# Kernel tuning notes

Hardware: AMD Instinct MI355X
Metric: run time of the kernel (lower is better)

The kernel has to match this reference:

```python
import jax, jax.numpy as jnp
import numpy as np

# Grid constants from init_kwargs: output_shape = [1, 10, 200, 176, 64]
D, H, W, C = 10, 200, 176, 64
N_VOX = 30000


def _conv_block(x, w, scale, bias, stride, pad):
    # x: [N,C,D,H,W]; w: [O,I,kd,kh,kw]; ZeroPad3d then valid Conv3d,
    # then fused (inference) BatchNorm3d + ReLU.
    x = jnp.pad(x, ((0, 0), (0, 0), (pad[0], pad[0]), (pad[1], pad[1]), (pad[2], pad[2])))
    x = jax.lax.conv_general_dilated(
        x, w, window_strides=stride, padding='VALID',
        dimension_numbers=('NCDHW', 'OIDHW', 'NCDHW'))
    s = scale[None, :, None, None, None]
    b = bias[None, :, None, None, None]
    return jax.nn.relu(x * s + b)


def setup_inputs() -> dict:
    key = jax.random.key(0)
    kf, kd, kh, kw, k1, k2, k3, ks = jax.random.split(key, 8)
    voxel_features = jax.random.normal(kf, (N_VOX, C), dtype=jnp.float32)
    # coors columns: (batch_idx, d, h, w) each in range
    b_idx = jnp.zeros((N_VOX,), dtype=jnp.int32)  # batch_size = 1
    d_idx = jax.random.randint(kd, (N_VOX,), 0, D, dtype=jnp.int32)
    h_idx = jax.random.randint(kh, (N_VOX,), 0, H, dtype=jnp.int32)
    w_idx = jax.random.randint(kw, (N_VOX,), 0, W, dtype=jnp.int32)
    coors = jnp.stack([b_idx, d_idx, h_idx, w_idx], axis=1)
    fan = 1.0 / np.sqrt(C * 27)
    W1 = jax.random.normal(k1, (64, C, 3, 3, 3), dtype=jnp.float32) * fan
    W2 = jax.random.normal(k2, (64, 64, 3, 3, 3), dtype=jnp.float32) * fan
    W3 = jax.random.normal(k3, (64, 64, 3, 3, 3), dtype=jnp.float32) * fan
    ks1, ks2, ks3 = jax.random.split(ks, 3)
    scale1 = jax.random.uniform(ks1, (64,), dtype=jnp.float32, minval=0.5, maxval=1.5)
    scale2 = jax.random.uniform(ks2, (64,), dtype=jnp.float32, minval=0.5, maxval=1.5)
    scale3 = jax.random.uniform(ks3, (64,), dtype=jnp.float32, minval=0.5, maxval=1.5)
    bias1 = jax.random.normal(jax.random.fold_in(ks1, 1), (64,), dtype=jnp.float32) * 0.1
    bias2 = jax.random.normal(jax.random.fold_in(ks2, 1), (64,), dtype=jnp.float32) * 0.1
    bias3 = jax.random.normal(jax.random.fold_in(ks3, 1), (64,), dtype=jnp.float32) * 0.1
    return {
        'voxel_features': voxel_features, 'coors': coors, 'batch_size': 1,
        'W1': W1, 'scale1': scale1, 'bias1': bias1,
        'W2': W2, 'scale2': scale2, 'bias2': bias2,
        'W3': W3, 'scale3': scale3, 'bias3': bias3,
    }


def reference(voxel_features, coors, batch_size,
              W1, scale1, bias1, W2, scale2, bias2, W3, scale3, bias3):
    # scatter_nd: sparse voxel features -> dense [B, D, H, W, C]
    dense = jnp.zeros((batch_size, D, H, W, C), dtype=voxel_features.dtype)
    dense = dense.at[coors[:, 0], coors[:, 1], coors[:, 2], coors[:, 3]].set(voxel_features)
    x = dense.transpose(0, 4, 1, 2, 3)  # [B, C, D, H, W]
    # middle_conv: Pad(1)+Conv3d s=(2,1,1); Pad(0,1,1)+Conv3d s=1; Pad(1)+Conv3d s=(2,1,1)
    x = _conv_block(x, W1, scale1, bias1, (2, 1, 1), (1, 1, 1))   # D: 10 -> 5
    x = _conv_block(x, W2, scale2, bias2, (1, 1, 1), (0, 1, 1))   # D: 5 -> 3
    x = _conv_block(x, W3, scale3, bias3, (2, 1, 1), (1, 1, 1))   # D: 3 -> 2
    N, Cc, Dd, Hh, Ww = x.shape
    return x.reshape(N, Cc * Dd, Hh, Ww)  # [B, 128, H, W]
```

## Files before the change

kernel.cpp:

```cpp
#include <hip/hip_runtime.h>
#include <cstddef>

#define HH 200
#define WW 176
#define HP 202
#define WP 178
#define D_IN 10
#define D1 5
#define D2 3
#define D3 2
#define SLICE ((size_t)HP * WP * 64)

#define LB_OFF 38912
#define LDS_TOTAL (38912 + 24576)

typedef _Float16 h8 __attribute__((ext_vector_type(8)));
typedef float f4 __attribute__((ext_vector_type(4)));

__device__ __forceinline__ void gl_lds16(const void* g, void* l) {
    __builtin_amdgcn_global_load_lds(
        (const __attribute__((address_space(1))) void*)g,
        (__attribute__((address_space(3))) void*)l, 16, 0, 0);
}

__global__ __launch_bounds__(256) void wtrans_k(const float* __restrict__ W1,
                                                const float* __restrict__ W2,
                                                const float* __restrict__ W3,
                                                _Float16* __restrict__ dst) {
    int idx = blockIdx.x * 256 + threadIdx.x;
    if (idx >= 3 * 27 * 64 * 64) return;
    int set = idx / (27 * 64 * 64);
    int r = idx - set * (27 * 64 * 64);
    const float* src = set == 0 ? W1 : (set == 1 ? W2 : W3);
    int ci = r & 63;
    int co = (r >> 6) & 63;
    int tap = r >> 12;
    int s = ci >> 3, j = ci & 7;
    dst[set * 110592 + tap * 4096 + co * 64 + (((s ^ (co & 7)) << 3) | j)] =
        (_Float16)src[(co * 64 + ci) * 27 + tap];
}

__global__ __launch_bounds__(256) void winner_k(const int* __restrict__ coors,
                                                int* __restrict__ winner, int nvox) {
    int v = blockIdx.x * 256 + threadIdx.x;
    if (v >= nvox) return;
    int d = coors[v * 4 + 1], h = coors[v * 4 + 2], w = coors[v * 4 + 3];
    atomicMax(&winner[(d * HH + h) * WW + w], v + 1);
}

__global__ __launch_bounds__(256) void scatter_k(const float* __restrict__ feat,
                                                 const int* __restrict__ coors,
                                                 const int* __restrict__ winner,
                                                 _Float16* __restrict__ A, int nvox) {
    int v = blockIdx.x * 4 + (threadIdx.x >> 6);
    int ci = threadIdx.x & 63;
    if (v >= nvox) return;
    int d = coors[v * 4 + 1], h = coors[v * 4 + 2], w = coors[v * 4 + 3];
    if (winner[(d * HH + h) * WW + w] != v + 1) return;
    int P = w + 1;
    int swz = (((ci >> 3) ^ (P & 7)) << 3) | (ci & 7);
    A[(size_t)d * SLICE + ((size_t)(h + 1) * WP + P) * 64 + swz] = (_Float16)feat[v * 64 + ci];
}

__global__ __launch_bounds__(256) void halo_k(_Float16* __restrict__ A2,
                                              _Float16* __restrict__ A3) {
    const int s = blockIdx.x;
    _Float16* base = (s < D1) ? (A2 + (size_t)s * SLICE) : (A3 + (size_t)(s - D1) * SLICE);
    const h8 z = {};
    for (int t = threadIdx.x; t < 6080; t += 256) {
        size_t off;
        if (t < 2848) {
            int r = t / 1424, c = t - r * 1424;
            off = (size_t)(r ? (HP - 1) : 0) * WP * 64 + (size_t)c * 8;
        } else {
            int u = t - 2848;
            int c = u / 1616, v = u - c * 1616;
            int hr = v >> 3, o = v & 7;
            off = ((size_t)hr * WP + (c ? (WP - 1) : 0)) * 64 + (size_t)o * 8;
        }
        *(h8*)(base + off) = z;
    }
}

template <int FINAL>
__global__ __launch_bounds__(256, 2) void conv_mfma_k(
    const _Float16* __restrict__ in, void* __restrict__ outp,
    const _Float16* __restrict__ wt,
    const float* __restrict__ scale, const float* __restrict__ bias,
    int inD, int strideD, int padD) {
    __shared__ char smem_raw[LDS_TOTAL];
    _Float16* smem = (_Float16*)smem_raw;

    const int lane = threadIdx.x & 63;
    const int wave = threadIdx.x >> 6;
    const int l16 = lane & 15;
    const int quad = lane >> 4;
    const int h0 = blockIdx.y * 4;
    const int wb = blockIdx.x * 48;
    const int d = blockIdx.z;

    f4 acc[3][4];
#pragma unroll
    for (int mt = 0; mt < 3; ++mt)
#pragma unroll
        for (int nt = 0; nt < 4; ++nt) acc[mt][nt] = (f4){0.f, 0.f, 0.f, 0.f};

    for (int kd = 0; kd < 3; ++kd) {
        const int zd = d * strideD + kd - padD;
        if (zd < 0 || zd >= inD) continue;
        const _Float16* __restrict__ aplane = in + (size_t)zd * SLICE;

        for (int kh = 0; kh < 3; ++kh) {
            __syncthreads();
            if (kh == 0) {
                for (int j = wave; j < 38; j += 4) {
                    int c = j * 64 + lane;
                    int r = c / 400;
                    int rem = c - r * 400;
                    if (r > 5) { r = 5; rem = c - 2000; }
                    int px = rem >> 3, s = rem & 7;
                    int g = wb + px;
                    if (g > 177) g = 177;
                    gl_lds16(aplane + ((size_t)(h0 + r) * WP + g) * 64 + s * 8,
                             smem_raw + j * 1024);
                }
            }
            {
                const _Float16* __restrict__ wrow = wt + (size_t)(kd * 9 + kh * 3) * 4096;
                for (int j = wave; j < 24; j += 4)
                    gl_lds16(wrow + (j * 64 + lane) * 8, smem_raw + LB_OFF + j * 1024);
            }
            __syncthreads();

#pragma unroll
            for (int kw = 0; kw < 3; ++kw) {
#pragma unroll
                for (int ch = 0; ch < 2; ++ch) {
                    const int q = ch * 4 + quad;
                    h8 b[4];
#pragma unroll
                    for (int nt = 0; nt < 4; ++nt)
                        b[nt] = *(const h8*)(smem + (LB_OFF / 2) + (kw * 64 + nt * 16 + l16) * 64 +
                                             ((q ^ (l16 & 7)) << 3));
#pragma unroll
                    for (int mt = 0; mt < 3; ++mt) {
                        const int px = mt * 16 + l16 + kw;
                        h8 a = *(const h8*)(smem + (wave + kh) * 3200 +
                                            px * 64 + ((q ^ (px & 7)) << 3));
#pragma unroll
                        for (int nt = 0; nt < 4; ++nt)
                            acc[mt][nt] = __builtin_amdgcn_mfma_f32_16x16x32_f16(
                                a, b[nt], acc[mt][nt], 0, 0, 0);
                    }
                }
            }
        }
    }

    const int h = h0 + wave;
#pragma unroll
    for (int nt = 0; nt < 4; ++nt) {
        const int co = nt * 16 + l16;
        const float s = scale[co];
        const float bb = bias[co];
#pragma unroll
        for (int mt = 0; mt < 3; ++mt) {
            const int w0 = wb + mt * 16 + quad * 4;
            if (w0 < WW) {
                if (FINAL) {
                    f4 v;
#pragma unroll
                    for (int r = 0; r < 4; ++r) {
                        float x = acc[mt][nt][r] * s + bb;
                        v[r] = x > 0.f ? x : 0.f;
                    }
                    *(f4*)((float*)outp + (((size_t)(co * 2 + d)) * HH + h) * WW + w0) = v;
                } else {
#pragma unroll
                    for (int r = 0; r < 4; ++r) {
                        float x = acc[mt][nt][r] * s + bb;
                        x = x > 0.f ? x : 0.f;
                        const int P = w0 + r + 1;
                        const int swz = (((co >> 3) ^ (P & 7)) << 3) | (co & 7);
                        ((_Float16*)outp)[(size_t)d * SLICE +
                            ((size_t)(h + 1) * WP + P) * 64 + swz] = (_Float16)x;
                    }
                }
            }
        }
    }
}

extern "C" void kernel_launch(void* const* d_in, const int* in_sizes, int n_in,
                              void* d_out, int out_size, void* d_ws, size_t ws_size,
                              hipStream_t stream) {
    const float* feat   = (const float*)d_in[0];
    const int*   coors  = (const int*)d_in[1];
    const float* W1     = (const float*)d_in[3];
    const float* scale1 = (const float*)d_in[4];
    const float* bias1  = (const float*)d_in[5];
    const float* W2     = (const float*)d_in[6];
    const float* scale2 = (const float*)d_in[7];
    const float* bias2  = (const float*)d_in[8];
    const float* W3     = (const float*)d_in[9];
    const float* scale3 = (const float*)d_in[10];
    const float* bias3  = (const float*)d_in[11];
    const int nvox = in_sizes[0] / 64;

    const size_t nA1 = (size_t)D_IN * SLICE;
    const size_t nWin = (size_t)D_IN * HH * WW;
    const size_t nA2 = (size_t)D1 * SLICE;
    const size_t nA3 = (size_t)D2 * SLICE;
    const size_t nWT = (size_t)27 * 64 * 64;

    _Float16* A1 = (_Float16*)d_ws;
    int* win = (int*)(A1 + nA1);
    _Float16* A2 = (_Float16*)(win + nWin);
    _Float16* A3 = A2 + nA2;
    _Float16* wt1 = A3 + nA3;
    _Float16* wt2 = wt1 + nWT;
    _Float16* wt3 = wt2 + nWT;

    hipMemsetAsync(d_ws, 0, nA1 * sizeof(_Float16) + nWin * sizeof(int), stream);
    halo_k<<<dim3(D1 + D2), 256, 0, stream>>>(A2, A3);

    const int nwt_blk = (3 * 27 * 64 * 64 + 255) / 256;
    wtrans_k<<<nwt_blk, 256, 0, stream>>>(W1, W2, W3, wt1);

    winner_k<<<(nvox + 255) / 256, 256, 0, stream>>>(coors, win, nvox);
    scatter_k<<<(nvox + 3) / 4, 256, 0, stream>>>(feat, coors, win, A1, nvox);

    dim3 blk(256);
    conv_mfma_k<0><<<dim3(4, 50, D1), blk, 0, stream>>>(A1, A2, wt1, scale1, bias1, D_IN, 2, 1);
    conv_mfma_k<0><<<dim3(4, 50, D2), blk, 0, stream>>>(A2, A3, wt2, scale2, bias2, D1, 1, 0);
    conv_mfma_k<1><<<dim3(4, 50, D3), blk, 0, stream>>>(A3, (float*)d_out, wt3, scale3, bias3, D2, 2, 1);
}
```

Baseline: 206.1 us.

## Double-buffer conv LDS stages with 8-wave blocks and merge prep kernels

The conv kernel now works on 8 output rows per 512-thread block. It loads its input rows and weight slices into two LDS buffers, so the next (kd, kh) stage is prefetched while MFMAs run on the current one, and the block needs only one barrier per stage. Depth taps that fall outside the input are skipped by computing kd bounds up front. The halo-zeroing, weight-transpose and winner kernels are merged into one launch to cut launch overhead. In exchange, A rows are reloaded for every kh rather than once per kd, and the block needs about 148 KB of dynamic LDS, which limits residency to one block per CU.

```diff
diff --git a/kernel.cpp b/kernel.cpp
--- a/kernel.cpp
+++ b/kernel.cpp
@@ -11,8 +11,10 @@
 #define D3 2
 #define SLICE ((size_t)HP * WP * 64)
 
-#define LB_OFF 38912
-#define LDS_TOTAL (38912 + 24576)
+#define LA_SZ 51200
+#define LB0   102400
+#define LB_SZ 24576
+#define LDS_TOTAL 151552
 
 typedef _Float16 h8 __attribute__((ext_vector_type(8)));
 typedef float f4 __attribute__((ext_vector_type(4)));
@@ -23,29 +25,51 @@
         (__attribute__((address_space(3))) void*)l, 16, 0, 0);
 }
 
-__global__ __launch_bounds__(256) void wtrans_k(const float* __restrict__ W1,
-                                                const float* __restrict__ W2,
-                                                const float* __restrict__ W3,
-                                                _Float16* __restrict__ dst) {
-    int idx = blockIdx.x * 256 + threadIdx.x;
-    if (idx >= 3 * 27 * 64 * 64) return;
-    int set = idx / (27 * 64 * 64);
-    int r = idx - set * (27 * 64 * 64);
-    const float* src = set == 0 ? W1 : (set == 1 ? W2 : W3);
-    int ci = r & 63;
-    int co = (r >> 6) & 63;
-    int tap = r >> 12;
-    int s = ci >> 3, j = ci & 7;
-    dst[set * 110592 + tap * 4096 + co * 64 + (((s ^ (co & 7)) << 3) | j)] =
-        (_Float16)src[(co * 64 + ci) * 27 + tap];
-}
-
-__global__ __launch_bounds__(256) void winner_k(const int* __restrict__ coors,
-                                                int* __restrict__ winner, int nvox) {
-    int v = blockIdx.x * 256 + threadIdx.x;
-    if (v >= nvox) return;
-    int d = coors[v * 4 + 1], h = coors[v * 4 + 2], w = coors[v * 4 + 3];
-    atomicMax(&winner[(d * HH + h) * WW + w], v + 1);
+__global__ __launch_bounds__(256) void prep_k(const float* __restrict__ W1,
+                                              const float* __restrict__ W2,
+                                              const float* __restrict__ W3,
+                                              _Float16* __restrict__ wdst,
+                                              _Float16* __restrict__ A2,
+                                              _Float16* __restrict__ A3,
+                                              const int* __restrict__ coors,
+                                              int* __restrict__ winner, int nvox) {
+    const int b = blockIdx.x;
+    if (b < 8) {
+        _Float16* base = (b < D1) ? (A2 + (size_t)b * SLICE) : (A3 + (size_t)(b - D1) * SLICE);
+        const h8 z = {};
+        for (int t = threadIdx.x; t < 6080; t += 256) {
+            size_t off;
+            if (t < 2848) {
+                int r = t / 1424, c = t - r * 1424;
+                off = (size_t)(r ? (HP - 1) : 0) * WP * 64 + (size_t)c * 8;
+            } else {
+                int u = t - 2848;
+                int c = u / 1616, v = u - c * 1616;
+                int hr = v >> 3, o = v & 7;
+                off = ((size_t)hr * WP + (c ? (WP - 1) : 0)) * 64 + (size_t)o * 8;
+            }
+            *(h8*)(base + off) = z;
+        }
+    } else if (b < 8 + 1296) {
+        int idx = (b - 8) * 256 + threadIdx.x;
+        if (idx < 3 * 27 * 64 * 64) {
+            int set = idx / 110592;
+            int r = idx - set * 110592;
+            const float* src = set == 0 ? W1 : (set == 1 ? W2 : W3);
+            int ci = r & 63;
+            int co = (r >> 6) & 63;
+            int tap = r >> 12;
+            int s = ci >> 3, j = ci & 7;
+            wdst[set * 110592 + tap * 4096 + co * 64 + (((s ^ (co & 7)) << 3) | j)] =
+                (_Float16)src[(co * 64 + ci) * 27 + tap];
+        }
+    } else {
+        int v = (b - 1304) * 256 + threadIdx.x;
+        if (v < nvox) {
+            int d = coors[v * 4 + 1], h = coors[v * 4 + 2], w = coors[v * 4 + 3];
+            atomicMax(&winner[(d * HH + h) * WW + w], v + 1);
+        }
+    }
 }
 
 __global__ __launch_bounds__(256) void scatter_k(const float* __restrict__ feat,
@@ -62,99 +86,81 @@
     A[(size_t)d * SLICE + ((size_t)(h + 1) * WP + P) * 64 + swz] = (_Float16)feat[v * 64 + ci];
 }
 
-__global__ __launch_bounds__(256) void halo_k(_Float16* __restrict__ A2,
-                                              _Float16* __restrict__ A3) {
-    const int s = blockIdx.x;
-    _Float16* base = (s < D1) ? (A2 + (size_t)s * SLICE) : (A3 + (size_t)(s - D1) * SLICE);
-    const h8 z = {};
-    for (int t = threadIdx.x; t < 6080; t += 256) {
-        size_t off;
-        if (t < 2848) {
-            int r = t / 1424, c = t - r * 1424;
-            off = (size_t)(r ? (HP - 1) : 0) * WP * 64 + (size_t)c * 8;
-        } else {
-            int u = t - 2848;
-            int c = u / 1616, v = u - c * 1616;
-            int hr = v >> 3, o = v & 7;
-            off = ((size_t)hr * WP + (c ? (WP - 1) : 0)) * 64 + (size_t)o * 8;
-        }
-        *(h8*)(base + off) = z;
-    }
-}
-
 template <int FINAL>
-__global__ __launch_bounds__(256, 2) void conv_mfma_k(
+__global__ __launch_bounds__(512, 2) void conv_mfma_k(
     const _Float16* __restrict__ in, void* __restrict__ outp,
     const _Float16* __restrict__ wt,
     const float* __restrict__ scale, const float* __restrict__ bias,
     int inD, int strideD, int padD) {
-    __shared__ char smem_raw[LDS_TOTAL];
-    _Float16* smem = (_Float16*)smem_raw;
+    extern __shared__ char smem[];
 
     const int lane = threadIdx.x & 63;
     const int wave = threadIdx.x >> 6;
     const int l16 = lane & 15;
     const int quad = lane >> 4;
-    const int h0 = blockIdx.y * 4;
+    const int h0 = blockIdx.y * 8;
     const int wb = blockIdx.x * 48;
     const int d = blockIdx.z;
 
+    int kd_lo = padD - d * strideD; if (kd_lo < 0) kd_lo = 0;
+    int kd_hi = inD - 1 - d * strideD + padD; if (kd_hi > 2) kd_hi = 2;
+    const int P = 3 * (kd_hi - kd_lo + 1);
+
+    auto stage = [&](int p, int par) {
+        const int kd = kd_lo + p / 3;
+        const int kh = p - 3 * (p / 3);
+        const int zd = d * strideD + kd - padD;
+        const _Float16* __restrict__ ap = in + (size_t)zd * SLICE;
+        char* la = smem + par * LA_SZ;
+        for (int j = wave; j < 50; j += 8) {
+            int c = j * 64 + lane;
+            int r = c / 400;
+            int rem = c - r * 400;
+            int px = rem >> 3, s = rem & 7;
+            int g = wb + px; if (g > 177) g = 177;
+            gl_lds16(ap + ((size_t)(h0 + kh + r) * WP + g) * 64 + s * 8, la + j * 1024);
+        }
+        const _Float16* __restrict__ wp = wt + (size_t)(kd * 9 + kh * 3) * 4096;
+        char* lb = smem + LB0 + par * LB_SZ;
+        for (int j = wave; j < 24; j += 8)
+            gl_lds16(wp + (j * 64 + lane) * 8, lb + j * 1024);
+    };
+
     f4 acc[3][4];
 #pragma unroll
     for (int mt = 0; mt < 3; ++mt)
 #pragma unroll
         for (int nt = 0; nt < 4; ++nt) acc[mt][nt] = (f4){0.f, 0.f, 0.f, 0.f};
 
-    for (int kd = 0; kd < 3; ++kd) {
-        const int zd = d * strideD + kd - padD;
-        if (zd < 0 || zd >= inD) continue;
-        const _Float16* __restrict__ aplane = in + (size_t)zd * SLICE;
-
-        for (int kh = 0; kh < 3; ++kh) {
-            __syncthreads();
-            if (kh == 0) {
-                for (int j = wave; j < 38; j += 4) {
-                    int c = j * 64 + lane;
-                    int r = c / 400;
-                    int rem = c - r * 400;
-                    if (r > 5) { r = 5; rem = c - 2000; }
-                    int px = rem >> 3, s = rem & 7;
-                    int g = wb + px;
-                    if (g > 177) g = 177;
-                    gl_lds16(aplane + ((size_t)(h0 + r) * WP + g) * 64 + s * 8,
-                             smem_raw + j * 1024);
+    stage(0, 0);
+    __syncthreads();
+
+    for (int p = 0; p < P; ++p) {
+        if (p + 1 < P) stage(p + 1, (p + 1) & 1);
+        const _Float16* la = (const _Float16*)(smem + (p & 1) * LA_SZ);
+        const _Float16* lb = (const _Float16*)(smem + LB0 + (p & 1) * LB_SZ);
+#pragma unroll
+        for (int kw = 0; kw < 3; ++kw) {
+#pragma unroll
+            for (int ch = 0; ch < 2; ++ch) {
+                const int q = ch * 4 + quad;
+                h8 b[4];
+#pragma unroll
+                for (int nt = 0; nt < 4; ++nt)
+                    b[nt] = *(const h8*)(lb + (kw * 64 + nt * 16 + l16) * 64 +
+                                         ((q ^ (l16 & 7)) << 3));
+#pragma unroll
+                for (int mt = 0; mt < 3; ++mt) {
+                    const int px = mt * 16 + l16 + kw;
+                    h8 a = *(const h8*)(la + (wave * 50 + px) * 64 + ((q ^ (px & 7)) << 3));
+#pragma unroll
+                    for (int nt = 0; nt < 4; ++nt)
+                        acc[mt][nt] = __builtin_amdgcn_mfma_f32_16x16x32_f16(
+                            a, b[nt], acc[mt][nt], 0, 0, 0);
                 }
             }
-            {
-                const _Float16* __restrict__ wrow = wt + (size_t)(kd * 9 + kh * 3) * 4096;
-                for (int j = wave; j < 24; j += 4)
-                    gl_lds16(wrow + (j * 64 + lane) * 8, smem_raw + LB_OFF + j * 1024);
-            }
-            __syncthreads();
-
-#pragma unroll
-            for (int kw = 0; kw < 3; ++kw) {
-#pragma unroll
-                for (int ch = 0; ch < 2; ++ch) {
-                    const int q = ch * 4 + quad;
-                    h8 b[4];
-#pragma unroll
-                    for (int nt = 0; nt < 4; ++nt)
-                        b[nt] = *(const h8*)(smem + (LB_OFF / 2) + (kw * 64 + nt * 16 + l16) * 64 +
-                                             ((q ^ (l16 & 7)) << 3));
-#pragma unroll
-                    for (int mt = 0; mt < 3; ++mt) {
-                        const int px = mt * 16 + l16 + kw;
-                        h8 a = *(const h8*)(smem + (wave + kh) * 3200 +
-                                            px * 64 + ((q ^ (px & 7)) << 3));
-#pragma unroll
-                        for (int nt = 0; nt < 4; ++nt)
-                            acc[mt][nt] = __builtin_amdgcn_mfma_f32_16x16x32_f16(
-                                a, b[nt], acc[mt][nt], 0, 0, 0);
-                    }
-                }
-            }
-        }
+        }
+        __syncthreads();
     }
 
     const int h = h0 + wave;
@@ -180,10 +186,10 @@
                     for (int r = 0; r < 4; ++r) {
                         float x = acc[mt][nt][r] * s + bb;
                         x = x > 0.f ? x : 0.f;
-                        const int P = w0 + r + 1;
-                        const int swz = (((co >> 3) ^ (P & 7)) << 3) | (co & 7);
+                        const int Pw = w0 + r + 1;
+                        const int swz = (((co >> 3) ^ (Pw & 7)) << 3) | (co & 7);
                         ((_Float16*)outp)[(size_t)d * SLICE +
-                            ((size_t)(h + 1) * WP + P) * 64 + swz] = (_Float16)x;
+                            ((size_t)(h + 1) * WP + Pw) * 64 + swz] = (_Float16)x;
                     }
                 }
             }
@@ -221,17 +227,20 @@
     _Float16* wt2 = wt1 + nWT;
     _Float16* wt3 = wt2 + nWT;
 
+    hipFuncSetAttribute((const void*)conv_mfma_k<0>,
+                        hipFuncAttributeMaxDynamicSharedMemorySize, LDS_TOTAL);
+    hipFuncSetAttribute((const void*)conv_mfma_k<1>,
+                        hipFuncAttributeMaxDynamicSharedMemorySize, LDS_TOTAL);
+
     hipMemsetAsync(d_ws, 0, nA1 * sizeof(_Float16) + nWin * sizeof(int), stream);
-    halo_k<<<dim3(D1 + D2), 256, 0, stream>>>(A2, A3);
-
-    const int nwt_blk = (3 * 27 * 64 * 64 + 255) / 256;
-    wtrans_k<<<nwt_blk, 256, 0, stream>>>(W1, W2, W3, wt1);
-
-    winner_k<<<(nvox + 255) / 256, 256, 0, stream>>>(coors, win, nvox);
+
+    const int win_blk = (nvox + 255) / 256;
+    prep_k<<<8 + 1296 + win_blk, 256, 0, stream>>>(W1, W2, W3, wt1, A2, A3,
+                                                   coors, win, nvox);
     scatter_k<<<(nvox + 3) / 4, 256, 0, stream>>>(feat, coors, win, A1, nvox);
 
-    dim3 blk(256);
-    conv_mfma_k<0><<<dim3(4, 50, D1), blk, 0, stream>>>(A1, A2, wt1, scale1, bias1, D_IN, 2, 1);
-    conv_mfma_k<0><<<dim3(4, 50, D2), blk, 0, stream>>>(A2, A3, wt2, scale2, bias2, D1, 1, 0);
-    conv_mfma_k<1><<<dim3(4, 50, D3), blk, 0, stream>>>(A3, (float*)d_out, wt3, scale3, bias3, D2, 2, 1);
-}
+    dim3 blk(512);
+    conv_mfma_k<0><<<dim3(4, 25, D1), blk, LDS_TOTAL, stream>>>(A1, A2, wt1, scale1, bias1, D_IN, 2, 1);
+    conv_mfma_k<0><<<dim3(4, 25, D2), blk, LDS_TOTAL, stream>>>(A2, A3, wt2, scale2, bias2, D1, 1, 0);
+    conv_mfma_k<1><<<dim3(4, 25, D3), blk, LDS_TOTAL, stream>>>(A3, (float*)d_out, wt3, scale3, bias3, D2, 2, 1);
+}
```

New measurement: 209.8 us. Within noise of the previous version (+1.8%).
